# Optimization experiments

Hardware: AMD Instinct MI355X
Metric: run time of the kernel (lower is better)

## Reference

```python
import jax, jax.numpy as jnp
import numpy as np

EMBED_DIM = 768
N_HEADS = 12
HEAD_SIZE = EMBED_DIM // N_HEADS
SCALE = HEAD_SIZE ** -0.5


def setup_inputs() -> dict:
    key = jax.random.key(0)
    k1, k2, k3, k4, k5 = jax.random.split(key, 5)
    B, T, C = 2, 4096, EMBED_DIM
    x = jax.random.normal(k1, (B, T, C), dtype=jnp.float32)
    # nn.Linear(embed_dim, 3*embed_dim): weight [3C, C], bias [3C]
    w_attn = jax.random.normal(k2, (3 * C, C), dtype=jnp.float32) * (C ** -0.5)
    b_attn = jax.random.normal(k3, (3 * C,), dtype=jnp.float32) * 0.02
    # nn.Linear(embed_dim, embed_dim)
    w_proj = jax.random.normal(k4, (C, C), dtype=jnp.float32) * (C ** -0.5)
    b_proj = jax.random.normal(k5, (C,), dtype=jnp.float32) * 0.02
    return {"x": x, "w_attn": w_attn, "b_attn": b_attn, "w_proj": w_proj, "b_proj": b_proj}


def reference(x, w_attn, b_attn, w_proj, b_proj):
    b, t, c = x.shape
    qkv = jnp.einsum('btc,dc->btd', x, w_attn) + b_attn  # [b,t,3c]
    q, k, v = jnp.split(qkv, 3, axis=-1)
    # [b, h, t, hs]
    q = q.reshape(b, t, N_HEADS, HEAD_SIZE).transpose(0, 2, 1, 3)
    k = k.reshape(b, t, N_HEADS, HEAD_SIZE).transpose(0, 2, 1, 3)
    v = v.reshape(b, t, N_HEADS, HEAD_SIZE).transpose(0, 2, 1, 3)
    scores = jnp.einsum('bhqd,bhkd->bhqk', q, k) * SCALE  # [b,h,t,t]
    causal = jnp.tril(jnp.ones((t, t), dtype=bool))
    scores = jnp.where(causal[None, None], scores, -jnp.inf)
    attn = jax.nn.softmax(scores, axis=-1)
    out = jnp.einsum('bhqk,bhkd->bhqd', attn, v)  # [b,h,t,hs]
    out = out.transpose(0, 2, 1, 3).reshape(b, t, c)
    out = jnp.einsum('btc,dc->btd', out, w_proj) + b_proj
    return out
```

## Files before the change

### kernel.cpp

```cpp
#include <hip/hip_runtime.h>
#include <hip/hip_bf16.h>

#define T_SEQ 4096
#define C_EMB 768
#define NH_ 12
#define HS_ 64
#define B_SZ 2
#define M_TOK 8192
#define N_QKV 2304

typedef __attribute__((ext_vector_type(8))) __bf16 bf16x8;
typedef __attribute__((ext_vector_type(8))) unsigned short ushort8v;
typedef __attribute__((ext_vector_type(2))) unsigned int uint2v;
typedef __attribute__((ext_vector_type(4))) unsigned int uint4v;
typedef __attribute__((ext_vector_type(4))) float f32x4;

__device__ __forceinline__ unsigned short f2bf(float f) {
  __hip_bfloat16 h = __float2bfloat16(f);
  return __builtin_bit_cast(unsigned short, h);
}

__device__ __forceinline__ unsigned int cvtpk(float lo, float hi) {
  unsigned int r;
  asm("v_cvt_pk_bf16_f32 %0, %1, %2" : "=v"(r) : "v"(lo), "v"(hi));
  return r;
}

__device__ __forceinline__ float fast_exp2(float x) {
  float r;
  asm("v_exp_f32 %0, %1" : "=v"(r) : "v"(x));
  return r;
}

#define KSWZ(row, bytecol) ((((row) * 128) + ((bytecol) ^ (((row) & 7) << 4))))

#define LOG2E 1.4426950408889634f

__global__ void cvt_f32_bf16(const float* __restrict__ in,
                             unsigned short* __restrict__ out) {
  int i = (blockIdx.x * 256 + threadIdx.x) * 8;
  float4 a = *reinterpret_cast<const float4*>(&in[i]);
  float4 b = *reinterpret_cast<const float4*>(&in[i + 4]);
  uint4v o;
  o.x = cvtpk(a.x, a.y);
  o.y = cvtpk(a.z, a.w);
  o.z = cvtpk(b.x, b.y);
  o.w = cvtpk(b.z, b.w);
  *reinterpret_cast<uint4v*>(&out[i]) = o;
}

template <int MODE>
__global__ __launch_bounds__(256) void gemm_bt_kernel(
    const unsigned short* __restrict__ A, const unsigned short* __restrict__ Bw,
    const float* __restrict__ bias, unsigned short* __restrict__ qo,
    unsigned short* __restrict__ ko, unsigned short* __restrict__ vo,
    float* __restrict__ fo, int Kdim, int Ndim) {
  __shared__ unsigned short as_[128 * 72];
  __shared__ unsigned short bs_[128 * 72];
  const int tid = threadIdx.x;
  const int lane = tid & 63;
  const int wid = tid >> 6;
  const int g = lane >> 4;
  const int l15 = lane & 15;
  const int m0 = blockIdx.y * 128;
  const int n0 = blockIdx.x * 128;
  const int wm = (wid >> 1) * 64;
  const int wn = (wid & 1) * 64;

  f32x4 acc[4][4];
#pragma unroll
  for (int i = 0; i < 4; ++i)
#pragma unroll
    for (int j = 0; j < 4; ++j) acc[i][j] = (f32x4){0.f, 0.f, 0.f, 0.f};

  for (int k0 = 0; k0 < Kdim; k0 += 64) {
#pragma unroll
    for (int it = 0; it < 4; ++it) {
      int cid = tid + it * 256;
      int r = cid >> 3, c8 = (cid & 7) << 3;
      *reinterpret_cast<ushort8v*>(&as_[r * 72 + c8]) =
          *reinterpret_cast<const ushort8v*>(&A[(size_t)(m0 + r) * Kdim + k0 + c8]);
      *reinterpret_cast<ushort8v*>(&bs_[r * 72 + c8]) =
          *reinterpret_cast<const ushort8v*>(&Bw[(size_t)(n0 + r) * Kdim + k0 + c8]);
    }
    __syncthreads();
#pragma unroll
    for (int ks = 0; ks < 2; ++ks) {
      bf16x8 af[4], bfr[4];
#pragma unroll
      for (int mf = 0; mf < 4; ++mf)
        af[mf] = __builtin_bit_cast(bf16x8,
            *reinterpret_cast<const ushort8v*>(&as_[(wm + mf * 16 + l15) * 72 + ks * 32 + g * 8]));
#pragma unroll
      for (int nf = 0; nf < 4; ++nf)
        bfr[nf] = __builtin_bit_cast(bf16x8,
            *reinterpret_cast<const ushort8v*>(&bs_[(wn + nf * 16 + l15) * 72 + ks * 32 + g * 8]));
#pragma unroll
      for (int mf = 0; mf < 4; ++mf)
#pragma unroll
        for (int nf = 0; nf < 4; ++nf)
          acc[mf][nf] = __builtin_amdgcn_mfma_f32_16x16x32_bf16(
              af[mf], bfr[nf], acc[mf][nf], 0, 0, 0);
    }
    __syncthreads();
  }

#pragma unroll
  for (int mf = 0; mf < 4; ++mf)
#pragma unroll
    for (int nf = 0; nf < 4; ++nf) {
      const int n = n0 + wn + nf * 16 + l15;
      const float bval = bias[n];
      float v4[4];
#pragma unroll
      for (int r2 = 0; r2 < 4; ++r2) v4[r2] = acc[mf][nf][r2] + bval;
      const int mb = m0 + wm + mf * 16 + g * 4;
      if (MODE == 1) {
#pragma unroll
        for (int r2 = 0; r2 < 4; ++r2)
          fo[(size_t)(mb + r2) * Ndim + n] = v4[r2];
      } else {
        const int which = (n >= 1536) ? 2 : ((n >= 768) ? 1 : 0);
        const int c = n - which * 768;
        const int h = c >> 6, d = c & 63;
        const int bI = mb >> 12, t = mb & 4095;
        if (which == 0) {
          const size_t off = ((size_t)(bI * NH_ + h) * T_SEQ + t) * HS_ + d;
#pragma unroll
          for (int r2 = 0; r2 < 4; ++r2)
            qo[off + (size_t)r2 * HS_] = f2bf(v4[r2] * 0.125f);
        } else if (which == 1) {
          const size_t off = ((size_t)(bI * NH_ + h) * T_SEQ + t) * HS_ + d;
#pragma unroll
          for (int r2 = 0; r2 < 4; ++r2)
            ko[off + (size_t)r2 * HS_] = f2bf(v4[r2]);
        } else {
          const size_t off = ((size_t)(bI * NH_ + h) * HS_ + d) * T_SEQ + t;
          uint2v o;
          o.x = cvtpk(v4[0], v4[1]);
          o.y = cvtpk(v4[2], v4[3]);
          *reinterpret_cast<uint2v*>(&vo[off]) = o;
        }
      }
    }
}

__global__ __launch_bounds__(256, 3) void flash_kernel(
    const unsigned short* __restrict__ Qg, const unsigned short* __restrict__ Kg,
    const unsigned short* __restrict__ Vtg, unsigned short* __restrict__ Og) {
  __shared__ __align__(16) char ksm[2][8192];
  __shared__ __align__(16) char vtm[2][8192];
  __shared__ __align__(16) char pls[16384];
  const int tid = threadIdx.x;
  const int lane = tid & 63;
  const int wid = tid >> 6;
  const int g = lane >> 4;
  const int l15 = lane & 15;

  const int cc = blockIdx.x & 255, kk = blockIdx.x >> 8;
  const int m = (kk == 0) ? (767 - cc) : ((kk == 1) ? (256 + cc) : cc);
  const int qt = m / 24;
  const int bh = m - qt * 24;
  const int q0 = qt * 128;
  const int b_ = bh / NH_, h_ = bh % NH_;
  const size_t kqbase = (size_t)bh * T_SEQ * HS_;
  const size_t vtbase = (size_t)bh * HS_ * T_SEQ;
  const int wq0 = wid * 32;

  bf16x8 qf[2][2];
#pragma unroll
  for (int nf = 0; nf < 2; ++nf)
#pragma unroll
    for (int ks = 0; ks < 2; ++ks)
      qf[nf][ks] = __builtin_bit_cast(bf16x8,
          *reinterpret_cast<const ushort8v*>(
              &Qg[kqbase + (size_t)(q0 + wq0 + nf * 16 + l15) * HS_ + ks * 32 + g * 8]));

  ushort8v ou;
#pragma unroll
  for (int j = 0; j < 8; ++j) ou[j] = 0x3f80;
  const bf16x8 ones_f = __builtin_bit_cast(bf16x8, ou);

  float m_run[2] = {-1e30f, -1e30f};
  float ml2[2] = {-1.4427e30f, -1.4427e30f};
  f32x4 oacc[2][4];
  f32x4 lacc[2];
#pragma unroll
  for (int nf = 0; nf < 2; ++nf) {
    lacc[nf] = (f32x4){0.f, 0.f, 0.f, 0.f};
#pragma unroll
    for (int j = 0; j < 4; ++j) oacc[nf][j] = (f32x4){0.f, 0.f, 0.f, 0.f};
  }

  char* pw = pls + wid * 4096;

  const int nkt = 2 * qt + 2;
  const int myt = ((q0 + wq0 + 31) >> 6) + 1;

  int sr[2], sc[2];
  const unsigned short* kgp[2];
  const unsigned short* vgp[2];
#pragma unroll
  for (int it = 0; it < 2; ++it) {
    int ci = tid + it * 256;
    sr[it] = ci >> 3;
    sc[it] = (ci & 7) * 16;
    kgp[it] = &Kg[kqbase + (size_t)sr[it] * HS_ + (sc[it] >> 1)];
    vgp[it] = &Vtg[vtbase + (size_t)sr[it] * T_SEQ + (sc[it] >> 1)];
  }

  ushort8v kreg[2], vreg[2];
#pragma unroll
  for (int it = 0; it < 2; ++it) {
    kreg[it] = *reinterpret_cast<const ushort8v*>(kgp[it]);
    vreg[it] = *reinterpret_cast<const ushort8v*>(vgp[it]);
  }
#pragma unroll
  for (int it = 0; it < 2; ++it) {
    *reinterpret_cast<ushort8v*>(&ksm[0][KSWZ(sr[it], sc[it])]) = kreg[it];
    *reinterpret_cast<ushort8v*>(&vtm[0][KSWZ(sr[it], sc[it])]) = vreg[it];
  }
  if (nkt > 1) {
#pragma unroll
    for (int it = 0; it < 2; ++it) {
      kreg[it] = *reinterpret_cast<const ushort8v*>(kgp[it] + (size_t)64 * HS_);
      vreg[it] = *reinterpret_cast<const ushort8v*>(vgp[it] + 64);
    }
  }

  for (int kt = 0; kt < nkt; ++kt) {
    __syncthreads();
    const int cur = kt & 1;
    if (kt + 1 < nkt) {
#pragma unroll
      for (int it = 0; it < 2; ++it) {
        *reinterpret_cast<ushort8v*>(&ksm[cur ^ 1][KSWZ(sr[it], sc[it])]) = kreg[it];
        *reinterpret_cast<ushort8v*>(&vtm[cur ^ 1][KSWZ(sr[it], sc[it])]) = vreg[it];
      }
      if (kt + 2 < nkt) {
        const int k2 = (kt + 2) << 6;
#pragma unroll
        for (int it = 0; it < 2; ++it) {
          kreg[it] = *reinterpret_cast<const ushort8v*>(kgp[it] + (size_t)k2 * HS_);
          vreg[it] = *reinterpret_cast<const ushort8v*>(vgp[it] + k2);
        }
      }
    }

    if (kt < myt) {
      const int k0 = kt << 6;
      const char* kb = ksm[cur];
      const char* vb = vtm[cur];

      f32x4 st[4][2];
#pragma unroll
      for (int i = 0; i < 4; ++i)
#pragma unroll
        for (int j = 0; j < 2; ++j) st[i][j] = (f32x4){0.f, 0.f, 0.f, 0.f};
#pragma unroll
      for (int ks = 0; ks < 2; ++ks) {
        bf16x8 kf[4];
#pragma unroll
        for (int mf = 0; mf < 4; ++mf)
          kf[mf] = __builtin_bit_cast(bf16x8,
              *reinterpret_cast<const ushort8v*>(
                  kb + KSWZ(mf * 16 + l15, ks * 64 + g * 16)));
#pragma unroll
        for (int mf = 0; mf < 4; ++mf)
#pragma unroll
          for (int nf = 0; nf < 2; ++nf)
            st[mf][nf] = __builtin_amdgcn_mfma_f32_16x16x32_bf16(
                kf[mf], qf[nf][ks], st[mf][nf], 0, 0, 0);
      }

      if (k0 + 63 > q0 + wq0) {
#pragma unroll
        for (int mf = 0; mf < 4; ++mf)
#pragma unroll
          for (int nf = 0; nf < 2; ++nf) {
            const int tq = q0 + wq0 + nf * 16 + l15;
#pragma unroll
            for (int r2 = 0; r2 < 4; ++r2) {
              const int tk = k0 + mf * 16 + g * 4 + r2;
              if (tk > tq) st[mf][nf][r2] = -1e30f;
            }
          }
      }

      float mx[2];
#pragma unroll
      for (int nf = 0; nf < 2; ++nf) {
        float v = fmaxf(fmaxf(st[0][nf][0], st[0][nf][1]),
                        fmaxf(st[0][nf][2], st[0][nf][3]));
        v = fmaxf(v, fmaxf(fmaxf(st[1][nf][0], st[1][nf][1]),
                           fmaxf(st[1][nf][2], st[1][nf][3])));
        v = fmaxf(v, fmaxf(fmaxf(st[2][nf][0], st[2][nf][1]),
                           fmaxf(st[2][nf][2], st[2][nf][3])));
        v = fmaxf(v, fmaxf(fmaxf(st[3][nf][0], st[3][nf][1]),
                           fmaxf(st[3][nf][2], st[3][nf][3])));
        v = fmaxf(v, __shfl_xor(v, 16));
        v = fmaxf(v, __shfl_xor(v, 32));
        mx[nf] = v;
      }
      if (__any((mx[0] > m_run[0] + 8.f) || (mx[1] > m_run[1] + 8.f))) {
#pragma unroll
        for (int nf = 0; nf < 2; ++nf) {
          const float mnew = fmaxf(m_run[nf], mx[nf]);
          const float alpha = fast_exp2((m_run[nf] - mnew) * LOG2E);
#pragma unroll
          for (int nd = 0; nd < 4; ++nd)
#pragma unroll
            for (int r2 = 0; r2 < 4; ++r2) oacc[nf][nd][r2] *= alpha;
#pragma unroll
          for (int r2 = 0; r2 < 4; ++r2) lacc[nf][r2] *= alpha;
          m_run[nf] = mnew;
          ml2[nf] = mnew * LOG2E;
        }
      }

#pragma unroll
      for (int mf = 0; mf < 4; ++mf)
#pragma unroll
        for (int nf = 0; nf < 2; ++nf) {
          const float p0 = fast_exp2(fmaf(st[mf][nf][0], LOG2E, -ml2[nf]));
          const float p1 = fast_exp2(fmaf(st[mf][nf][1], LOG2E, -ml2[nf]));
          const float p2 = fast_exp2(fmaf(st[mf][nf][2], LOG2E, -ml2[nf]));
          const float p3 = fast_exp2(fmaf(st[mf][nf][3], LOG2E, -ml2[nf]));
          uint2v w;
          w.x = cvtpk(p0, p1);
          w.y = cvtpk(p2, p3);
          *reinterpret_cast<uint2v*>(
              pw + KSWZ(nf * 16 + l15, mf * 32 + g * 8)) = w;
        }

#pragma unroll
      for (int ks = 0; ks < 2; ++ks) {
        bf16x8 pf[2];
#pragma unroll
        for (int nf = 0; nf < 2; ++nf)
          pf[nf] = __builtin_bit_cast(bf16x8,
              *reinterpret_cast<const ushort8v*>(
                  pw + KSWZ(nf * 16 + l15, ks * 64 + g * 16)));
        bf16x8 vt[4];
#pragma unroll
        for (int nd = 0; nd < 4; ++nd)
          vt[nd] = __builtin_bit_cast(bf16x8,
              *reinterpret_cast<const ushort8v*>(
                  vb + KSWZ(nd * 16 + l15, ks * 64 + g * 16)));
#pragma unroll
        for (int nf = 0; nf < 2; ++nf) {
#pragma unroll
          for (int nd = 0; nd < 4; ++nd)
            oacc[nf][nd] = __builtin_amdgcn_mfma_f32_16x16x32_bf16(
                vt[nd], pf[nf], oacc[nf][nd], 0, 0, 0);
          lacc[nf] = __builtin_amdgcn_mfma_f32_16x16x32_bf16(
              ones_f, pf[nf], lacc[nf], 0, 0, 0);
        }
      }
    }
  }

#pragma unroll
  for (int nf = 0; nf < 2; ++nf) {
    const float invl = 1.f / lacc[nf][0];
    const int t = q0 + wq0 + nf * 16 + l15;
#pragma unroll
    for (int nd = 0; nd < 4; ++nd) {
      uint2v o;
      o.x = cvtpk(oacc[nf][nd][0] * invl, oacc[nf][nd][1] * invl);
      o.y = cvtpk(oacc[nf][nd][2] * invl, oacc[nf][nd][3] * invl);
      *reinterpret_cast<uint2v*>(
          &Og[((size_t)(b_ * T_SEQ + t)) * C_EMB + h_ * 64 + nd * 16 + g * 4]) = o;
    }
  }
}

extern "C" void kernel_launch(void* const* d_in, const int* in_sizes, int n_in,
                              void* d_out, int out_size, void* d_ws, size_t ws_size,
                              hipStream_t stream) {
  const float* x = (const float*)d_in[0];
  const float* w_attn = (const float*)d_in[1];
  const float* b_attn = (const float*)d_in[2];
  const float* w_proj = (const float*)d_in[3];
  const float* b_proj = (const float*)d_in[4];
  float* out = (float*)d_out;

  char* ws = (char*)d_ws;
  size_t off = 0;
  auto carve = [&](size_t bytes) -> void* {
    void* p = ws + off;
    off += (bytes + 255) & ~(size_t)255;
    return p;
  };
  unsigned short* xbf = (unsigned short*)carve((size_t)M_TOK * C_EMB * 2);
  unsigned short* wab = (unsigned short*)carve((size_t)N_QKV * C_EMB * 2);
  unsigned short* wpb = (unsigned short*)carve((size_t)C_EMB * C_EMB * 2);
  unsigned short* Qb = (unsigned short*)carve((size_t)B_SZ * NH_ * T_SEQ * HS_ * 2);
  unsigned short* Kb = (unsigned short*)carve((size_t)B_SZ * NH_ * T_SEQ * HS_ * 2);
  unsigned short* Vtb = (unsigned short*)carve((size_t)B_SZ * NH_ * T_SEQ * HS_ * 2);
  unsigned short* Ob = (unsigned short*)carve((size_t)M_TOK * C_EMB * 2);

  cvt_f32_bf16<<<3072, 256, 0, stream>>>(x, xbf);
  cvt_f32_bf16<<<864, 256, 0, stream>>>(w_attn, wab);
  cvt_f32_bf16<<<288, 256, 0, stream>>>(w_proj, wpb);

  gemm_bt_kernel<0><<<dim3(N_QKV / 128, M_TOK / 128), 256, 0, stream>>>(
      xbf, wab, b_attn, Qb, Kb, Vtb, nullptr, C_EMB, N_QKV);

  flash_kernel<<<dim3(768), 256, 0, stream>>>(Qb, Kb, Vtb, Ob);

  gemm_bt_kernel<1><<<dim3(C_EMB / 128, M_TOK / 128), 256, 0, stream>>>(
      Ob, wpb, b_proj, nullptr, nullptr, nullptr, out, C_EMB, C_EMB);
}
```

Baseline: 169.3 us.

## Stage GEMM and attention tiles with direct global-to-LDS loads and swizzle

Replaces register-staged global loads plus LDS stores with buffer global_load_lds (16-byte direct-to-LDS) in both the QKV/proj GEMM and the flash-attention K/V pipeline. The GEMM's padded shared layout becomes an XOR-swizzled 128-byte-row layout matching the per-lane source-column permutation. This frees VGPRs and removes LDS write instructions. It also adds s_setprio around MFMA blocks and trims the lacc rescale to one element. Correctness relies on the direct-LDS writes being complete at the barrier, and staging the next tile right after the barrier changes how much load latency overlaps with compute.

After: 174.3 us. 3.0% more time.

```diff
diff --git a/kernel.cpp b/kernel.cpp
--- a/kernel.cpp
+++ b/kernel.cpp
@@ -31,6 +31,11 @@
   asm("v_exp_f32 %0, %1" : "=v"(r) : "v"(x));
   return r;
 }
+
+#define GLOAD_LDS16(gp, lp)                                                   \
+  __builtin_amdgcn_global_load_lds(                                           \
+      (const __attribute__((address_space(1))) void*)(gp),                    \
+      (__attribute__((address_space(3))) void*)(lp), 16, 0, 0)
 
 #define KSWZ(row, bytecol) ((((row) * 128) + ((bytecol) ^ (((row) & 7) << 4))))
 
@@ -55,8 +60,8 @@
     const float* __restrict__ bias, unsigned short* __restrict__ qo,
     unsigned short* __restrict__ ko, unsigned short* __restrict__ vo,
     float* __restrict__ fo, int Kdim, int Ndim) {
-  __shared__ unsigned short as_[128 * 72];
-  __shared__ unsigned short bs_[128 * 72];
+  __shared__ __align__(16) char as_[16384];
+  __shared__ __align__(16) char bs_[16384];
   const int tid = threadIdx.x;
   const int lane = tid & 63;
   const int wid = tid >> 6;
@@ -67,6 +72,9 @@
   const int wm = (wid >> 1) * 64;
   const int wn = (wid & 1) * 64;
 
+  const int lrow = lane >> 3;
+  const int scol = ((lane & 7) ^ lrow) * 8;
+
   f32x4 acc[4][4];
 #pragma unroll
   for (int i = 0; i < 4; ++i)
@@ -75,26 +83,29 @@
 
   for (int k0 = 0; k0 < Kdim; k0 += 64) {
 #pragma unroll
-    for (int it = 0; it < 4; ++it) {
-      int cid = tid + it * 256;
-      int r = cid >> 3, c8 = (cid & 7) << 3;
-      *reinterpret_cast<ushort8v*>(&as_[r * 72 + c8]) =
-          *reinterpret_cast<const ushort8v*>(&A[(size_t)(m0 + r) * Kdim + k0 + c8]);
-      *reinterpret_cast<ushort8v*>(&bs_[r * 72 + c8]) =
-          *reinterpret_cast<const ushort8v*>(&Bw[(size_t)(n0 + r) * Kdim + k0 + c8]);
+    for (int i = 0; i < 4; ++i) {
+      const int r = wid * 32 + i * 8 + lrow;
+      GLOAD_LDS16(&A[(size_t)(m0 + r) * Kdim + k0 + scol],
+                  as_ + wid * 4096 + i * 1024);
+      GLOAD_LDS16(&Bw[(size_t)(n0 + r) * Kdim + k0 + scol],
+                  bs_ + wid * 4096 + i * 1024);
     }
     __syncthreads();
 #pragma unroll
     for (int ks = 0; ks < 2; ++ks) {
       bf16x8 af[4], bfr[4];
 #pragma unroll
-      for (int mf = 0; mf < 4; ++mf)
+      for (int mf = 0; mf < 4; ++mf) {
+        const int ra = wm + mf * 16 + l15;
         af[mf] = __builtin_bit_cast(bf16x8,
-            *reinterpret_cast<const ushort8v*>(&as_[(wm + mf * 16 + l15) * 72 + ks * 32 + g * 8]));
-#pragma unroll
-      for (int nf = 0; nf < 4; ++nf)
+            *reinterpret_cast<const ushort8v*>(as_ + KSWZ(ra, ks * 64 + g * 16)));
+      }
+#pragma unroll
+      for (int nf = 0; nf < 4; ++nf) {
+        const int rb = wn + nf * 16 + l15;
         bfr[nf] = __builtin_bit_cast(bf16x8,
-            *reinterpret_cast<const ushort8v*>(&bs_[(wn + nf * 16 + l15) * 72 + ks * 32 + g * 8]));
+            *reinterpret_cast<const ushort8v*>(bs_ + KSWZ(rb, ks * 64 + g * 16)));
+      }
 #pragma unroll
       for (int mf = 0; mf < 4; ++mf)
 #pragma unroll
@@ -197,55 +208,26 @@
   const int nkt = 2 * qt + 2;
   const int myt = ((q0 + wq0 + 31) >> 6) + 1;
 
-  int sr[2], sc[2];
-  const unsigned short* kgp[2];
-  const unsigned short* vgp[2];
-#pragma unroll
-  for (int it = 0; it < 2; ++it) {
-    int ci = tid + it * 256;
-    sr[it] = ci >> 3;
-    sc[it] = (ci & 7) * 16;
-    kgp[it] = &Kg[kqbase + (size_t)sr[it] * HS_ + (sc[it] >> 1)];
-    vgp[it] = &Vtg[vtbase + (size_t)sr[it] * T_SEQ + (sc[it] >> 1)];
-  }
-
-  ushort8v kreg[2], vreg[2];
-#pragma unroll
-  for (int it = 0; it < 2; ++it) {
-    kreg[it] = *reinterpret_cast<const ushort8v*>(kgp[it]);
-    vreg[it] = *reinterpret_cast<const ushort8v*>(vgp[it]);
-  }
-#pragma unroll
-  for (int it = 0; it < 2; ++it) {
-    *reinterpret_cast<ushort8v*>(&ksm[0][KSWZ(sr[it], sc[it])]) = kreg[it];
-    *reinterpret_cast<ushort8v*>(&vtm[0][KSWZ(sr[it], sc[it])]) = vreg[it];
-  }
-  if (nkt > 1) {
-#pragma unroll
-    for (int it = 0; it < 2; ++it) {
-      kreg[it] = *reinterpret_cast<const ushort8v*>(kgp[it] + (size_t)64 * HS_);
-      vreg[it] = *reinterpret_cast<const ushort8v*>(vgp[it] + 64);
-    }
-  }
+  const int lrow = lane >> 3;
+  const int scol = ((lane & 7) ^ lrow) * 8;
+
+  auto stage = [&](int buf, int kt) {
+#pragma unroll
+    for (int i = 0; i < 2; ++i) {
+      const int r = wid * 16 + i * 8 + lrow;
+      GLOAD_LDS16(&Kg[kqbase + (size_t)(kt * 64 + r) * HS_ + scol],
+                  ksm[buf] + wid * 2048 + i * 1024);
+      GLOAD_LDS16(&Vtg[vtbase + (size_t)r * T_SEQ + kt * 64 + scol],
+                  vtm[buf] + wid * 2048 + i * 1024);
+    }
+  };
+
+  stage(0, 0);
 
   for (int kt = 0; kt < nkt; ++kt) {
     __syncthreads();
     const int cur = kt & 1;
-    if (kt + 1 < nkt) {
-#pragma unroll
-      for (int it = 0; it < 2; ++it) {
-        *reinterpret_cast<ushort8v*>(&ksm[cur ^ 1][KSWZ(sr[it], sc[it])]) = kreg[it];
-        *reinterpret_cast<ushort8v*>(&vtm[cur ^ 1][KSWZ(sr[it], sc[it])]) = vreg[it];
-      }
-      if (kt + 2 < nkt) {
-        const int k2 = (kt + 2) << 6;
-#pragma unroll
-        for (int it = 0; it < 2; ++it) {
-          kreg[it] = *reinterpret_cast<const ushort8v*>(kgp[it] + (size_t)k2 * HS_);
-          vreg[it] = *reinterpret_cast<const ushort8v*>(vgp[it] + k2);
-        }
-      }
-    }
+    if (kt + 1 < nkt) stage(cur ^ 1, kt + 1);
 
     if (kt < myt) {
       const int k0 = kt << 6;
@@ -257,6 +239,7 @@
       for (int i = 0; i < 4; ++i)
 #pragma unroll
         for (int j = 0; j < 2; ++j) st[i][j] = (f32x4){0.f, 0.f, 0.f, 0.f};
+      __builtin_amdgcn_s_setprio(1);
 #pragma unroll
       for (int ks = 0; ks < 2; ++ks) {
         bf16x8 kf[4];
@@ -272,6 +255,7 @@
             st[mf][nf] = __builtin_amdgcn_mfma_f32_16x16x32_bf16(
                 kf[mf], qf[nf][ks], st[mf][nf], 0, 0, 0);
       }
+      __builtin_amdgcn_s_setprio(0);
 
       if (k0 + 63 > q0 + wq0) {
 #pragma unroll
@@ -311,8 +295,7 @@
           for (int nd = 0; nd < 4; ++nd)
 #pragma unroll
             for (int r2 = 0; r2 < 4; ++r2) oacc[nf][nd][r2] *= alpha;
-#pragma unroll
-          for (int r2 = 0; r2 < 4; ++r2) lacc[nf][r2] *= alpha;
+          lacc[nf][0] *= alpha;
           m_run[nf] = mnew;
           ml2[nf] = mnew * LOG2E;
         }
@@ -333,6 +316,7 @@
               pw + KSWZ(nf * 16 + l15, mf * 32 + g * 8)) = w;
         }
 
+      __builtin_amdgcn_s_setprio(1);
 #pragma unroll
       for (int ks = 0; ks < 2; ++ks) {
         bf16x8 pf[2];
@@ -357,6 +341,7 @@
               ones_f, pf[nf], lacc[nf], 0, 0, 0);
         }
       }
+      __builtin_amdgcn_s_setprio(0);
     }
   }
 
```
